# Performance work log

Hardware: AMD Instinct MI355X
Metric: run time of the kernel (lower is better)

The kernel has to match this reference:

```python
import jax, jax.numpy as jnp
import numpy as np

N = 100000      # nodes
E = 800000      # edges
F_IN = 256      # input feature dim
HID = 256       # hidden_channels
H = 8           # heads
C = HID // H    # per-head dim = 32
OUT = 128       # out_channels
EPS_BN = 1e-5
NEG_SLOPE = 0.2


def _segment_softmax(logits, seg, n):
    # logits: [E, H], softmax over edges sharing the same destination node
    m = jax.ops.segment_max(logits, seg, num_segments=n)          # [N, H]
    m = jnp.where(jnp.isfinite(m), m, 0.0)                         # nodes with no in-edges
    ex = jnp.exp(logits - m[seg])                                  # [E, H]
    denom = jax.ops.segment_sum(ex, seg, num_segments=n)          # [N, H]
    return ex / (denom[seg] + 1e-16)


def _gatv2_layer(x, src, dst, Wl, bl, Wr, br, att, bias):
    # PyG GATv2Conv (eval, concat=True): lin_l on source, lin_r on target
    n = x.shape[0]
    xl = (x @ Wl + bl).reshape(n, H, C)   # [N, H, C]
    xr = (x @ Wr + br).reshape(n, H, C)   # [N, H, C]
    e = jax.nn.leaky_relu(xl[src] + xr[dst], NEG_SLOPE)            # [E, H, C]
    logits = jnp.einsum('ehc,hc->eh', e, att)                      # [E, H]
    alpha = _segment_softmax(logits, dst, n)                       # [E, H]
    msg = xl[src] * alpha[:, :, None]                              # [E, H, C]
    out = jax.ops.segment_sum(msg, dst, num_segments=n)            # [N, H, C]
    return out.reshape(n, H * C) + bias


def _batchnorm(x, gamma, beta):
    # training-mode batch statistics (deterministic), biased variance
    mu = x.mean(axis=0)
    var = x.var(axis=0)
    return gamma * (x - mu) * jax.lax.rsqrt(var + EPS_BN) + beta


def setup_inputs() -> dict:
    key = jax.random.key(0)
    ks = jax.random.split(key, 12)
    s = 0.05
    z = jnp.zeros
    o = jnp.ones
    rn = lambda k, shp: jax.random.normal(k, shp, jnp.float32) * s
    return {
        'x': jax.random.normal(ks[0], (N, F_IN), jnp.float32),
        'edge_index': jax.random.randint(ks[1], (2, E), 0, N, jnp.int32),
        'Wl1': rn(ks[2], (F_IN, HID)), 'bl1': z((HID,), jnp.float32),
        'Wr1': rn(ks[3], (F_IN, HID)), 'br1': z((HID,), jnp.float32),
        'att1': rn(ks[4], (H, C)), 'bias1': z((HID,), jnp.float32),
        'gamma1': o((HID,), jnp.float32), 'beta1': z((HID,), jnp.float32),
        'Wl2': rn(ks[5], (HID, HID)), 'bl2': z((HID,), jnp.float32),
        'Wr2': rn(ks[6], (HID, HID)), 'br2': z((HID,), jnp.float32),
        'att2': rn(ks[7], (H, C)), 'bias2': z((HID,), jnp.float32),
        'gamma2': o((HID,), jnp.float32), 'beta2': z((HID,), jnp.float32),
        'Wfc': rn(ks[8], (HID, OUT)), 'bfc': z((OUT,), jnp.float32),
    }


def reference(x, edge_index, Wl1, bl1, Wr1, br1, att1, bias1, gamma1, beta1,
              Wl2, bl2, Wr2, br2, att2, bias2, gamma2, beta2, Wfc, bfc):
    src, dst = edge_index[0], edge_index[1]
    h = _gatv2_layer(x, src, dst, Wl1, bl1, Wr1, br1, att1, bias1)
    h = jax.nn.elu(_batchnorm(h, gamma1, beta1))
    h = _gatv2_layer(h, src, dst, Wl2, bl2, Wr2, br2, att2, bias2)
    h = jax.nn.elu(_batchnorm(h, gamma2, beta2))
    h = h @ Wfc + bfc
    # F.normalize(p=2, dim=-1)
    norm = jnp.maximum(jnp.linalg.norm(h, axis=-1, keepdims=True), 1e-12)
    return h / norm
```

## Files before the change

### kernel.cpp

```cpp
#include <hip/hip_runtime.h>
#include <math.h>

#define N_NODES 100000
#define N_EDGES 800000
#define NPAD    100096
#define FDIM 256
#define HEADS 8
#define CDIM 32
#define OUTF 128

#define SCAN_BLOCK 256
#define SCAN_NBLK ((N_NODES + SCAN_BLOCK - 1) / SCAN_BLOCK)

typedef _Float16 f16x2 __attribute__((ext_vector_type(2)));
typedef _Float16 f16x8 __attribute__((ext_vector_type(8)));
typedef float  f32x4 __attribute__((ext_vector_type(4)));
typedef unsigned short u16;

__device__ __forceinline__ u16 f2h(float f) {
    union { _Float16 h; u16 u; } c;
    c.h = (_Float16)f;
    return c.u;
}
__device__ __forceinline__ float h2f(u16 u) {
    union { u16 u; _Float16 h; } c;
    c.u = u;
    return (float)c.h;
}
__device__ __forceinline__ f16x2 u2h2(unsigned u) {
    return __builtin_bit_cast(f16x2, u);
}

__device__ __forceinline__ void gload_lds16(const void* g, void* l) {
    __builtin_amdgcn_global_load_lds((const __attribute__((address_space(1))) void*)g,
                                     (__attribute__((address_space(3))) void*)l, 16, 0, 0);
}

__global__ void cast_half(const float* __restrict__ src, int n_valid4, int n_pad4,
                          u16* __restrict__ dst) {
    int i = blockIdx.x * blockDim.x + threadIdx.x;
    int stride = gridDim.x * blockDim.x;
    for (; i < n_pad4; i += stride) {
        f32x4 v = {0.f, 0.f, 0.f, 0.f};
        if (i < n_valid4) v = ((const f32x4*)src)[i];
        ((ushort4*)dst)[i] = make_ushort4(f2h(v[0]), f2h(v[1]), f2h(v[2]), f2h(v[3]));
    }
}

__global__ void prep_w_layer(const float* __restrict__ Wl, const float* __restrict__ Wr,
                             u16* __restrict__ Wt) {
    int idx = blockIdx.x * blockDim.x + threadIdx.x;
    if (idx >= 512 * 256) return;
    int n = idx >> 8, k = idx & 255;
    float w = (n < 256) ? Wl[k * 256 + n] : Wr[k * 256 + (n - 256)];
    Wt[idx] = f2h(w);
}

__global__ void prep_w_fc(const float* __restrict__ Wfc, u16* __restrict__ Wt) {
    int idx = blockIdx.x * blockDim.x + threadIdx.x;
    if (idx >= 128 * 256) return;
    int n = idx >> 8, k = idx & 255;
    Wt[idx] = f2h(Wfc[k * 128 + n]);
}

template <bool HOUT, int NS>
__global__ __launch_bounds__(256) void gemm_h(
        const u16* __restrict__ A, const u16* __restrict__ Wt,
        const float* __restrict__ bias0, const float* __restrict__ bias1,
        void* __restrict__ C0v, void* __restrict__ C1v, int ldc, int M) {
    __shared__ __align__(16) u16 lA[128 * 64];
    __shared__ __align__(16) u16 lB[128 * 64];

    int tid = threadIdx.x;
    int wid = tid >> 6, lane = tid & 63;
    int wm = wid >> 1, wn = wid & 1;
    int lr = lane & 15, lk = lane >> 4;

    int orig = blockIdx.x;
    int nwg = gridDim.x;
    int q = nwg >> 3, r = nwg & 7;
    int xcd = orig & 7, loc = orig >> 3;
    int swz = (xcd < r) ? (xcd * (q + 1) + loc) : (r * (q + 1) + (xcd - r) * q + loc);
    int m0 = (swz / NS) * 128;
    int n0 = (swz % NS) * 128;

    f32x4 acc[4][4] = {};

#pragma unroll 1
    for (int k0 = 0; k0 < 256; k0 += 64) {
#pragma unroll
        for (int i = 0; i < 4; i++) {
            int t = i * 256 + tid;
            int row = t >> 3;
            int ch = (t & 7) ^ (row & 7);
            gload_lds16(A + (size_t)(m0 + row) * 256 + k0 + ch * 8,
                        (char*)lA + i * 4096 + wid * 1024);
        }
#pragma unroll
        for (int i = 0; i < 4; i++) {
            int t = i * 256 + tid;
            int row = t >> 3;
            int ch = (t & 7) ^ (row & 7);
            gload_lds16(Wt + (size_t)(n0 + row) * 256 + k0 + ch * 8,
                        (char*)lB + i * 4096 + wid * 1024);
        }
        __syncthreads();

#pragma unroll
        for (int kk = 0; kk < 2; kk++) {
            f16x8 af[4], bf[4];
#pragma unroll
            for (int mr = 0; mr < 4; mr++) {
                int rr = wm * 64 + mr * 16 + lr;
                int qq = (kk * 4 + lk) ^ (rr & 7);
                af[mr] = *(const f16x8*)&lA[rr * 64 + qq * 8];
            }
#pragma unroll
            for (int nr = 0; nr < 4; nr++) {
                int rr = wn * 64 + nr * 16 + lr;
                int qq = (kk * 4 + lk) ^ (rr & 7);
                bf[nr] = *(const f16x8*)&lB[rr * 64 + qq * 8];
            }
#pragma unroll
            for (int mr = 0; mr < 4; mr++)
#pragma unroll
                for (int nr = 0; nr < 4; nr++)
                    acc[mr][nr] = __builtin_amdgcn_mfma_f32_16x16x32_f16(
                        af[mr], bf[nr], acc[mr][nr], 0, 0, 0);
        }
        __syncthreads();
    }

#pragma unroll
    for (int mr = 0; mr < 4; mr++) {
#pragma unroll
        for (int nr = 0; nr < 4; nr++) {
            int col = n0 + wn * 64 + nr * 16 + lr;
            void* Cp; const float* bp; int c;
            if (col < 256) { Cp = C0v; bp = bias0; c = col; }
            else           { Cp = C1v; bp = bias1; c = col - 256; }
            float b = bp[c];
#pragma unroll
            for (int j = 0; j < 4; j++) {
                int row = m0 + wm * 64 + mr * 16 + lk * 4 + j;
                if (row < M) {
                    float v = acc[mr][nr][j] + b;
                    if constexpr (HOUT)
                        ((u16*)Cp)[(size_t)row * ldc + c] = f2h(v);
                    else
                        ((float*)Cp)[(size_t)row * ldc + c] = v;
                }
            }
        }
    }
}

__global__ void count_deg(const int* __restrict__ dstA, int* __restrict__ deg) {
    int i = blockIdx.x * blockDim.x + threadIdx.x;
    int stride = gridDim.x * blockDim.x;
    for (; i < N_EDGES; i += stride) atomicAdd(&deg[dstA[i]], 1);
}

__global__ void scan_phase1(const int* __restrict__ deg, int* __restrict__ blocksum) {
    __shared__ int sdata[SCAN_BLOCK];
    int i = blockIdx.x * SCAN_BLOCK + threadIdx.x;
    sdata[threadIdx.x] = (i < N_NODES) ? deg[i] : 0;
    __syncthreads();
    for (int off = SCAN_BLOCK / 2; off > 0; off >>= 1) {
        if (threadIdx.x < off) sdata[threadIdx.x] += sdata[threadIdx.x + off];
        __syncthreads();
    }
    if (threadIdx.x == 0) blocksum[blockIdx.x] = sdata[0];
}

__global__ void scan_phase2(int* __restrict__ blocksum) {
    __shared__ int part[512];
    int t = threadIdx.x;
    int v = (t < SCAN_NBLK) ? blocksum[t] : 0;
    part[t] = v;
    __syncthreads();
    for (int off = 1; off < 512; off <<= 1) {
        int u = 0;
        if (t >= off) u = part[t - off];
        __syncthreads();
        if (t >= off) part[t] += u;
        __syncthreads();
    }
    if (t < SCAN_NBLK) blocksum[t] = part[t] - v;
}

__global__ void scan_phase3(const int* __restrict__ deg, const int* __restrict__ blockoff,
                            int* __restrict__ rowstart, int* __restrict__ cursor) {
    __shared__ int part[SCAN_BLOCK];
    int t = threadIdx.x;
    int i = blockIdx.x * SCAN_BLOCK + t;
    int v = (i < N_NODES) ? deg[i] : 0;
    part[t] = v;
    __syncthreads();
    for (int off = 1; off < SCAN_BLOCK; off <<= 1) {
        int u = 0;
        if (t >= off) u = part[t - off];
        __syncthreads();
        if (t >= off) part[t] += u;
        __syncthreads();
    }
    if (i < N_NODES) {
        int excl = blockoff[blockIdx.x] + part[t] - v;
        rowstart[i] = excl;
        cursor[i] = excl;
        if (i == N_NODES - 1) rowstart[N_NODES] = blockoff[blockIdx.x] + part[t];
    }
}

__global__ void fill_csr(const int* __restrict__ srcA, const int* __restrict__ dstA,
                         int* __restrict__ cursor, int* __restrict__ csr_src) {
    int i = blockIdx.x * blockDim.x + threadIdx.x;
    int stride = gridDim.x * blockDim.x;
    for (; i < N_EDGES; i += stride) {
        int pos = atomicAdd(&cursor[dstA[i]], 1);
        csr_src[pos] = srcA[i];
    }
}

__global__ void gat_fused(const u16* __restrict__ xl, const u16* __restrict__ xr,
                          const int* __restrict__ rowstart, const int* __restrict__ csr_src,
                          const float* __restrict__ att, u16* __restrict__ out) {
    int wid = (blockIdx.x * blockDim.x + threadIdx.x) >> 6;
    int lane = threadIdx.x & 63;
    if (wid >= N_NODES) return;
    int hl = lane & 31;
    int up = lane >> 5;
    int c0 = hl * 8;

    uint4 xru = *(const uint4*)(xr + (size_t)wid * FDIM + c0);
    f16x2 xr0 = u2h2(xru.x), xr1 = u2h2(xru.y), xr2 = u2h2(xru.z), xr3 = u2h2(xru.w);
    f32x4 av0 = *(const f32x4*)(att + c0);
    f32x4 av1 = *(const f32x4*)(att + c0 + 4);
    f16x2 a0 = {(_Float16)av0[0], (_Float16)av0[1]};
    f16x2 a1 = {(_Float16)av0[2], (_Float16)av0[3]};
    f16x2 a2 = {(_Float16)av1[0], (_Float16)av1[1]};
    f16x2 a3 = {(_Float16)av1[2], (_Float16)av1[3]};
    const f16x2 k02 = {(_Float16)0.2f, (_Float16)0.2f};

    float acc[8] = {0.f, 0.f, 0.f, 0.f, 0.f, 0.f, 0.f, 0.f};
    float den = 0.f;

    int jb = rowstart[wid], je = rowstart[wid + 1];
    if (jb < je) {
        int jlast = je - 1;
        int nsteps = (je - jb + 1) >> 1;
        int i0 = jb + up;     if (i0 > jlast) i0 = jlast;
        uint4 u0 = *(const uint4*)(xl + (size_t)csr_src[i0] * FDIM + c0);
        int i1 = jb + 2 + up; if (i1 > jlast) i1 = jlast;
        uint4 u1 = *(const uint4*)(xl + (size_t)csr_src[i1] * FDIM + c0);

        for (int t = 0; t < nsteps; ++t) {
            int in_ = jb + 2 * t + 4 + up; if (in_ > jlast) in_ = jlast;
            uint4 un = *(const uint4*)(xl + (size_t)csr_src[in_] * FDIM + c0);

            int myidx = jb + 2 * t + up;
            f16x2 x0 = u2h2(u0.x), x1 = u2h2(u0.y), x2 = u2h2(u0.z), x3 = u2h2(u0.w);
            f16x2 v0 = x0 + xr0, v1 = x1 + xr1, v2 = x2 + xr2, v3 = x3 + xr3;
            f16x2 t0 = __builtin_elementwise_max(v0, v0 * k02);
            f16x2 t1 = __builtin_elementwise_max(v1, v1 * k02);
            f16x2 t2 = __builtin_elementwise_max(v2, v2 * k02);
            f16x2 t3 = __builtin_elementwise_max(v3, v3 * k02);
            float s = __builtin_amdgcn_fdot2(t0, a0, 0.f, false);
            s = __builtin_amdgcn_fdot2(t1, a1, s, false);
            s = __builtin_amdgcn_fdot2(t2, a2, s, false);
            s = __builtin_amdgcn_fdot2(t3, a3, s, false);
            s += __shfl_xor(s, 1);
            s += __shfl_xor(s, 2);
            float e = (myidx <= jlast) ? __expf(s) : 0.f;
            den += e;
            acc[0] += e * (float)x0[0]; acc[1] += e * (float)x0[1];
            acc[2] += e * (float)x1[0]; acc[3] += e * (float)x1[1];
            acc[4] += e * (float)x2[0]; acc[5] += e * (float)x2[1];
            acc[6] += e * (float)x3[0]; acc[7] += e * (float)x3[1];
            u0 = u1; u1 = un;
        }
    }
    den += __shfl_xor(den, 32);
#pragma unroll
    for (int i = 0; i < 8; i++) acc[i] += __shfl_xor(acc[i], 32);

    if (up == 0) {
        float inv = 1.f / (den + 1e-16f);
        u16 h[8];
#pragma unroll
        for (int i = 0; i < 8; i++) h[i] = f2h(acc[i] * inv);
        *(uint4*)(out + (size_t)wid * FDIM + c0) = *(const uint4*)h;
    }
}

__global__ void bn_stats_h(const u16* __restrict__ X, float* __restrict__ sum,
                           float* __restrict__ sumsq, int nrows) {
    int col = threadIdx.x;
    float s = 0.f, ss = 0.f;
    for (int r = blockIdx.x; r < nrows; r += gridDim.x) {
        float v = h2f(X[(size_t)r * FDIM + col]);
        s += v;
        ss += v * v;
    }
    atomicAdd(&sum[col], s);
    atomicAdd(&sumsq[col], ss);
}

__global__ void bn_finalize(const float* __restrict__ sum, const float* __restrict__ sumsq,
                            const float* __restrict__ gamma, const float* __restrict__ beta,
                            float* __restrict__ scale, float* __restrict__ shift) {
    int c = threadIdx.x;
    float mean = sum[c] * (1.f / N_NODES);
    float var = sumsq[c] * (1.f / N_NODES) - mean * mean;
    float sc = gamma[c] * rsqrtf(var + 1e-5f);
    scale[c] = sc;
    shift[c] = beta[c] - mean * sc;
}

__global__ void bn_elu_h(const u16* __restrict__ X, const float* __restrict__ scale,
                         const float* __restrict__ shift, u16* __restrict__ dst) {
    int i = blockIdx.x * blockDim.x + threadIdx.x;
    int stride = gridDim.x * blockDim.x;
    const int n_valid4 = N_NODES * FDIM / 4;
    const int n_pad4 = NPAD * FDIM / 4;
    for (; i < n_pad4; i += stride) {
        u16 h[4] = {0, 0, 0, 0};
        if (i < n_valid4) {
            ushort4 v = ((const ushort4*)X)[i];
            int c0 = (i * 4) & (FDIM - 1);
            float f0 = h2f(v.x) * scale[c0 + 0] + shift[c0 + 0];
            float f1 = h2f(v.y) * scale[c0 + 1] + shift[c0 + 1];
            float f2 = h2f(v.z) * scale[c0 + 2] + shift[c0 + 2];
            float f3 = h2f(v.w) * scale[c0 + 3] + shift[c0 + 3];
            f0 = f0 > 0.f ? f0 : expf(f0) - 1.f;
            f1 = f1 > 0.f ? f1 : expf(f1) - 1.f;
            f2 = f2 > 0.f ? f2 : expf(f2) - 1.f;
            f3 = f3 > 0.f ? f3 : expf(f3) - 1.f;
            h[0] = f2h(f0); h[1] = f2h(f1); h[2] = f2h(f2); h[3] = f2h(f3);
        }
        ((ushort4*)dst)[i] = make_ushort4(h[0], h[1], h[2], h[3]);
    }
}

__global__ void l2norm(float* __restrict__ Y, int nrows) {
    int gtid = blockIdx.x * blockDim.x + threadIdx.x;
    int wave = gtid >> 6;
    int lane = threadIdx.x & 63;
    int nwaves = (gridDim.x * blockDim.x) >> 6;
    for (int r = wave; r < nrows; r += nwaves) {
        float v0 = Y[(size_t)r * OUTF + lane];
        float v1 = Y[(size_t)r * OUTF + 64 + lane];
        float ss = v0 * v0 + v1 * v1;
        ss += __shfl_xor(ss, 32);
        ss += __shfl_xor(ss, 16);
        ss += __shfl_xor(ss, 8);
        ss += __shfl_xor(ss, 4);
        ss += __shfl_xor(ss, 2);
        ss += __shfl_xor(ss, 1);
        float inv = 1.f / fmaxf(sqrtf(ss), 1e-12f);
        Y[(size_t)r * OUTF + lane] = v0 * inv;
        Y[(size_t)r * OUTF + 64 + lane] = v1 * inv;
    }
}

extern "C" void kernel_launch(void* const* d_in, const int* in_sizes, int n_in,
                              void* d_out, int out_size, void* d_ws, size_t ws_size,
                              hipStream_t stream) {
    const float* x     = (const float*)d_in[0];
    const int*   ei    = (const int*)d_in[1];
    const float* Wl1   = (const float*)d_in[2];
    const float* bl1   = (const float*)d_in[3];
    const float* Wr1   = (const float*)d_in[4];
    const float* br1   = (const float*)d_in[5];
    const float* att1  = (const float*)d_in[6];
    const float* gamma1 = (const float*)d_in[8];
    const float* beta1  = (const float*)d_in[9];
    const float* Wl2   = (const float*)d_in[10];
    const float* bl2   = (const float*)d_in[11];
    const float* Wr2   = (const float*)d_in[12];
    const float* br2   = (const float*)d_in[13];
    const float* att2  = (const float*)d_in[14];
    const float* gamma2 = (const float*)d_in[16];
    const float* beta2  = (const float*)d_in[17];
    const float* Wfc   = (const float*)d_in[18];
    const float* bfc   = (const float*)d_in[19];

    const int* srcA = ei;
    const int* dstA = ei + N_EDGES;

    const size_t REG = (size_t)NPAD * FDIM * 4;
    char* p = (char*)d_ws;
    char* R0 = p;            p += REG;
    char* R1 = p;            p += REG;
    char* R2 = p;            p += REG;
    u16* WTH   = (u16*)p;              p += 512 * 256 * 2;
    float* SUM = (float*)p;            p += FDIM * 4;
    float* SQ  = (float*)p;            p += FDIM * 4;
    float* SC  = (float*)p;            p += FDIM * 4;
    float* SH  = (float*)p;            p += FDIM * 4;
    int* DEG      = (int*)p;           p += (size_t)N_NODES * 4;
    int* ROWSTART = (int*)p;           p += (size_t)(N_NODES + 1) * 4;
    int* CURSOR   = (int*)p;           p += (size_t)N_NODES * 4;
    int* CSR      = (int*)p;           p += (size_t)N_EDGES * 4;
    int* BLKSUM   = (int*)p;           p += (size_t)SCAN_NBLK * 4;

    const int gat_grid = (N_NODES + 3) / 4;
    const int gemm_grid_layer = (NPAD / 128) * 4;
    const int gemm_grid_fc = NPAD / 128;

    hipMemsetAsync(DEG, 0, (size_t)N_NODES * sizeof(int), stream);
    count_deg<<<2048, 256, 0, stream>>>(dstA, DEG);
    scan_phase1<<<SCAN_NBLK, SCAN_BLOCK, 0, stream>>>(DEG, BLKSUM);
    scan_phase2<<<1, 512, 0, stream>>>(BLKSUM);
    scan_phase3<<<SCAN_NBLK, SCAN_BLOCK, 0, stream>>>(DEG, BLKSUM, ROWSTART, CURSOR);
    fill_csr<<<2048, 256, 0, stream>>>(srcA, dstA, CURSOR, CSR);

    cast_half<<<4096, 256, 0, stream>>>(x, N_NODES * FDIM / 4, NPAD * FDIM / 4, (u16*)R0);
    prep_w_layer<<<512, 256, 0, stream>>>(Wl1, Wr1, WTH);
    gemm_h<true, 4><<<gemm_grid_layer, 256, 0, stream>>>((u16*)R0, WTH, bl1, br1, R1, R2, 256, N_NODES);
    gat_fused<<<gat_grid, 256, 0, stream>>>((u16*)R1, (u16*)R2, ROWSTART, CSR, att1, (u16*)R0);

    hipMemsetAsync(SUM, 0, 2 * FDIM * sizeof(float), stream);
    bn_stats_h<<<1024, 256, 0, stream>>>((u16*)R0, SUM, SQ, N_NODES);
    bn_finalize<<<1, 256, 0, stream>>>(SUM, SQ, gamma1, beta1, SC, SH);
    bn_elu_h<<<2048, 256, 0, stream>>>((u16*)R0, SC, SH, (u16*)R1);

    prep_w_layer<<<512, 256, 0, stream>>>(Wl2, Wr2, WTH);
    gemm_h<true, 4><<<gemm_grid_layer, 256, 0, stream>>>((u16*)R1, WTH, bl2, br2, R2, R0, 256, N_NODES);
    gat_fused<<<gat_grid, 256, 0, stream>>>((u16*)R2, (u16*)R0, ROWSTART, CSR, att2, (u16*)R1);

    hipMemsetAsync(SUM, 0, 2 * FDIM * sizeof(float), stream);
    bn_stats_h<<<1024, 256, 0, stream>>>((u16*)R1, SUM, SQ, N_NODES);
    bn_finalize<<<1, 256, 0, stream>>>(SUM, SQ, gamma2, beta2, SC, SH);
    bn_elu_h<<<2048, 256, 0, stream>>>((u16*)R1, SC, SH, (u16*)R2);

    prep_w_fc<<<128, 256, 0, stream>>>(Wfc, WTH);
    gemm_h<false, 1><<<gemm_grid_fc, 256, 0, stream>>>((u16*)R2, WTH, bfc, bfc, d_out, d_out, 128, N_NODES);
    l2norm<<<2048, 256, 0, stream>>>((float*)d_out, N_NODES);
}
```

Baseline: 636.5 us.

## Fuse L2 normalization into FC GEMM epilogue and load weights directly to registers

The final FC GEMM now computes per-row sums of squares through shared-memory atomics and writes normalized output, which removes the separate l2norm kernel and its read-modify-write pass over the output. Separately, the GEMM stops staging the weight tile in LDS and has each wave load its B fragments straight from global memory into registers. That cuts LDS traffic and usage but adds redundant, less coalesced global loads of the weights, and both layer GEMMs are affected. The shared-memory atomics in the epilogue add some contention.

```diff
diff --git a/kernel.cpp b/kernel.cpp
--- a/kernel.cpp
+++ b/kernel.cpp
@@ -63,13 +63,13 @@
     Wt[idx] = f2h(Wfc[k * 128 + n]);
 }
 
-template <bool HOUT, int NS>
+template <bool HOUT, int NS, bool L2N>
 __global__ __launch_bounds__(256) void gemm_h(
         const u16* __restrict__ A, const u16* __restrict__ Wt,
         const float* __restrict__ bias0, const float* __restrict__ bias1,
         void* __restrict__ C0v, void* __restrict__ C1v, int ldc, int M) {
     __shared__ __align__(16) u16 lA[128 * 64];
-    __shared__ __align__(16) u16 lB[128 * 64];
+    __shared__ float rssq[128];
 
     int tid = threadIdx.x;
     int wid = tid >> 6, lane = tid & 63;
@@ -88,6 +88,13 @@
 
 #pragma unroll 1
     for (int k0 = 0; k0 < 256; k0 += 64) {
+        f16x8 bf[4][2];
+#pragma unroll
+        for (int nr = 0; nr < 4; nr++)
+#pragma unroll
+            for (int kk = 0; kk < 2; kk++)
+                bf[nr][kk] = *(const f16x8*)&Wt[(size_t)(n0 + wn * 64 + nr * 16 + lr) * 256
+                                                + k0 + kk * 32 + lk * 8];
 #pragma unroll
         for (int i = 0; i < 4; i++) {
             int t = i * 256 + tid;
@@ -96,19 +103,11 @@
             gload_lds16(A + (size_t)(m0 + row) * 256 + k0 + ch * 8,
                         (char*)lA + i * 4096 + wid * 1024);
         }
-#pragma unroll
-        for (int i = 0; i < 4; i++) {
-            int t = i * 256 + tid;
-            int row = t >> 3;
-            int ch = (t & 7) ^ (row & 7);
-            gload_lds16(Wt + (size_t)(n0 + row) * 256 + k0 + ch * 8,
-                        (char*)lB + i * 4096 + wid * 1024);
-        }
         __syncthreads();
 
 #pragma unroll
         for (int kk = 0; kk < 2; kk++) {
-            f16x8 af[4], bf[4];
+            f16x8 af[4];
 #pragma unroll
             for (int mr = 0; mr < 4; mr++) {
                 int rr = wm * 64 + mr * 16 + lr;
@@ -116,42 +115,75 @@
                 af[mr] = *(const f16x8*)&lA[rr * 64 + qq * 8];
             }
 #pragma unroll
-            for (int nr = 0; nr < 4; nr++) {
-                int rr = wn * 64 + nr * 16 + lr;
-                int qq = (kk * 4 + lk) ^ (rr & 7);
-                bf[nr] = *(const f16x8*)&lB[rr * 64 + qq * 8];
-            }
-#pragma unroll
             for (int mr = 0; mr < 4; mr++)
 #pragma unroll
                 for (int nr = 0; nr < 4; nr++)
                     acc[mr][nr] = __builtin_amdgcn_mfma_f32_16x16x32_f16(
-                        af[mr], bf[nr], acc[mr][nr], 0, 0, 0);
+                        af[mr], bf[nr][kk], acc[mr][nr], 0, 0, 0);
         }
         __syncthreads();
     }
 
 #pragma unroll
-    for (int mr = 0; mr < 4; mr++) {
+    for (int mr = 0; mr < 4; mr++)
 #pragma unroll
         for (int nr = 0; nr < 4; nr++) {
             int col = n0 + wn * 64 + nr * 16 + lr;
-            void* Cp; const float* bp; int c;
-            if (col < 256) { Cp = C0v; bp = bias0; c = col; }
-            else           { Cp = C1v; bp = bias1; c = col - 256; }
-            float b = bp[c];
+            float b = (col < 256) ? bias0[col] : bias1[col - 256];
+#pragma unroll
+            for (int j = 0; j < 4; j++) acc[mr][nr][j] += b;
+        }
+
+    if constexpr (L2N) {
+        if (tid < 128) rssq[tid] = 0.f;
+        __syncthreads();
+#pragma unroll
+        for (int mr = 0; mr < 4; mr++)
 #pragma unroll
             for (int j = 0; j < 4; j++) {
-                int row = m0 + wm * 64 + mr * 16 + lk * 4 + j;
+                int rl = wm * 64 + mr * 16 + lk * 4 + j;
+                float s = 0.f;
+#pragma unroll
+                for (int nr = 0; nr < 4; nr++) s += acc[mr][nr][j] * acc[mr][nr][j];
+                atomicAdd(&rssq[rl], s);
+            }
+        __syncthreads();
+#pragma unroll
+        for (int mr = 0; mr < 4; mr++)
+#pragma unroll
+            for (int j = 0; j < 4; j++) {
+                int rl = wm * 64 + mr * 16 + lk * 4 + j;
+                int row = m0 + rl;
                 if (row < M) {
-                    float v = acc[mr][nr][j] + b;
-                    if constexpr (HOUT)
-                        ((u16*)Cp)[(size_t)row * ldc + c] = f2h(v);
-                    else
-                        ((float*)Cp)[(size_t)row * ldc + c] = v;
+                    float inv = 1.f / fmaxf(sqrtf(rssq[rl]), 1e-12f);
+#pragma unroll
+                    for (int nr = 0; nr < 4; nr++) {
+                        int col = n0 + wn * 64 + nr * 16 + lr;
+                        ((float*)C0v)[(size_t)row * ldc + col] = acc[mr][nr][j] * inv;
+                    }
                 }
             }
-        }
+    } else {
+#pragma unroll
+        for (int mr = 0; mr < 4; mr++)
+#pragma unroll
+            for (int nr = 0; nr < 4; nr++) {
+                int col = n0 + wn * 64 + nr * 16 + lr;
+                void* Cp; int c;
+                if (col < 256) { Cp = C0v; c = col; }
+                else           { Cp = C1v; c = col - 256; }
+#pragma unroll
+                for (int j = 0; j < 4; j++) {
+                    int row = m0 + wm * 64 + mr * 16 + lk * 4 + j;
+                    if (row < M) {
+                        float v = acc[mr][nr][j];
+                        if constexpr (HOUT)
+                            ((u16*)Cp)[(size_t)row * ldc + c] = f2h(v);
+                        else
+                            ((float*)Cp)[(size_t)row * ldc + c] = v;
+                    }
+                }
+            }
     }
 }
 
@@ -342,27 +374,6 @@
     }
 }
 
-__global__ void l2norm(float* __restrict__ Y, int nrows) {
-    int gtid = blockIdx.x * blockDim.x + threadIdx.x;
-    int wave = gtid >> 6;
-    int lane = threadIdx.x & 63;
-    int nwaves = (gridDim.x * blockDim.x) >> 6;
-    for (int r = wave; r < nrows; r += nwaves) {
-        float v0 = Y[(size_t)r * OUTF + lane];
-        float v1 = Y[(size_t)r * OUTF + 64 + lane];
-        float ss = v0 * v0 + v1 * v1;
-        ss += __shfl_xor(ss, 32);
-        ss += __shfl_xor(ss, 16);
-        ss += __shfl_xor(ss, 8);
-        ss += __shfl_xor(ss, 4);
-        ss += __shfl_xor(ss, 2);
-        ss += __shfl_xor(ss, 1);
-        float inv = 1.f / fmaxf(sqrtf(ss), 1e-12f);
-        Y[(size_t)r * OUTF + lane] = v0 * inv;
-        Y[(size_t)r * OUTF + 64 + lane] = v1 * inv;
-    }
-}
-
 extern "C" void kernel_launch(void* const* d_in, const int* in_sizes, int n_in,
                               void* d_out, int out_size, void* d_ws, size_t ws_size,
                               hipStream_t stream) {
@@ -417,7 +428,7 @@
 
     cast_half<<<4096, 256, 0, stream>>>(x, N_NODES * FDIM / 4, NPAD * FDIM / 4, (u16*)R0);
     prep_w_layer<<<512, 256, 0, stream>>>(Wl1, Wr1, WTH);
-    gemm_h<true, 4><<<gemm_grid_layer, 256, 0, stream>>>((u16*)R0, WTH, bl1, br1, R1, R2, 256, N_NODES);
+    gemm_h<true, 4, false><<<gemm_grid_layer, 256, 0, stream>>>((u16*)R0, WTH, bl1, br1, R1, R2, 256, N_NODES);
     gat_fused<<<gat_grid, 256, 0, stream>>>((u16*)R1, (u16*)R2, ROWSTART, CSR, att1, (u16*)R0);
 
     hipMemsetAsync(SUM, 0, 2 * FDIM * sizeof(float), stream);
@@ -426,7 +437,7 @@
     bn_elu_h<<<2048, 256, 0, stream>>>((u16*)R0, SC, SH, (u16*)R1);
 
     prep_w_layer<<<512, 256, 0, stream>>>(Wl2, Wr2, WTH);
-    gemm_h<true, 4><<<gemm_grid_layer, 256, 0, stream>>>((u16*)R1, WTH, bl2, br2, R2, R0, 256, N_NODES);
+    gemm_h<true, 4, false><<<gemm_grid_layer, 256, 0, stream>>>((u16*)R1, WTH, bl2, br2, R2, R0, 256, N_NODES);
     gat_fused<<<gat_grid, 256, 0, stream>>>((u16*)R2, (u16*)R0, ROWSTART, CSR, att2, (u16*)R1);
 
     hipMemsetAsync(SUM, 0, 2 * FDIM * sizeof(float), stream);
@@ -435,6 +446,5 @@
     bn_elu_h<<<2048, 256, 0, stream>>>((u16*)R1, SC, SH, (u16*)R2);
 
     prep_w_fc<<<128, 256, 0, stream>>>(Wfc, WTH);
-    gemm_h<false, 1><<<gemm_grid_fc, 256, 0, stream>>>((u16*)R2, WTH, bfc, bfc, d_out, d_out, 128, N_NODES);
-    l2norm<<<2048, 256, 0, stream>>>((float*)d_out, N_NODES);
-}
+    gemm_h<false, 1, true><<<gemm_grid_fc, 256, 0, stream>>>((u16*)R2, WTH, bfc, bfc, d_out, d_out, 128, N_NODES);
+}
```

Result: slower. 696.7 us (+9.5%).
